# Kernel optimization log

Measured on AMD Instinct MI355X. Metric: run time of the kernel, lower is better.

## Reference

```python
import jax, jax.numpy as jnp
import numpy as np

N = 100000   # nodes
F = 512      # in_channels
H = 128      # hidden_channels
HEADS = 2
E = 1600000  # edges
C = 64       # out_channels (classes)
EPS = 1e-5
GW = 0.8     # graph_weight


def setup_inputs() -> dict:
    key = jax.random.key(0)
    ks = jax.random.split(key, 16)
    rn = lambda k, s: jax.random.normal(k, s, jnp.float32) * 0.05
    return {
        'x': jax.random.normal(ks[0], (N, F), jnp.float32),
        'edge_index': jax.random.randint(ks[1], (2, E), 0, N),
        # TransConv params
        't_fc_w': rn(ks[2], (F, H)), 't_fc_b': jnp.zeros((H,), jnp.float32),
        't_ln0_g': jnp.ones((H,), jnp.float32), 't_ln0_b': jnp.zeros((H,), jnp.float32),
        't_wq_w': rn(ks[3], (H, H * HEADS)), 't_wq_b': jnp.zeros((H * HEADS,), jnp.float32),
        't_wk_w': rn(ks[4], (H, H * HEADS)), 't_wk_b': jnp.zeros((H * HEADS,), jnp.float32),
        't_wv_w': rn(ks[5], (H, H * HEADS)), 't_wv_b': jnp.zeros((H * HEADS,), jnp.float32),
        't_ln1_g': jnp.ones((H,), jnp.float32), 't_ln1_b': jnp.zeros((H,), jnp.float32),
        # GraphConv params
        'g_fc_w': rn(ks[6], (F, H)), 'g_fc_b': jnp.zeros((H,), jnp.float32),
        'g_bn0_g': jnp.ones((H,), jnp.float32), 'g_bn0_b': jnp.zeros((H,), jnp.float32),
        'g_conv_w': rn(ks[7], (H, H)), 'g_conv_b': jnp.zeros((H,), jnp.float32),
        'g_bn1_g': jnp.ones((H,), jnp.float32), 'g_bn1_b': jnp.zeros((H,), jnp.float32),
        # output fc
        'fc_w': rn(ks[8], (H, C)), 'fc_b': jnp.zeros((C,), jnp.float32),
    }


def _layernorm(x, g, b):
    mu = jnp.mean(x, axis=-1, keepdims=True)
    var = jnp.mean((x - mu) ** 2, axis=-1, keepdims=True)
    return (x - mu) * jax.lax.rsqrt(var + EPS) * g + b


def _batchnorm_eval(x, g, b):
    # eval-mode BN right after reset: running_mean=0, running_var=1
    return x * (1.0 / np.sqrt(1.0 + EPS)) * g + b


def _trans_conv(x, fc_w, fc_b, ln0_g, ln0_b, wq_w, wq_b, wk_w, wk_b, wv_w, wv_b, ln1_g, ln1_b):
    h = jax.nn.relu(_layernorm(x @ fc_w + fc_b, ln0_g, ln0_b))
    x0 = h
    n = h.shape[0]
    qs = (h @ wq_w + wq_b).reshape(n, HEADS, H)
    ks = (h @ wk_w + wk_b).reshape(n, HEADS, H)
    vs = (h @ wv_w + wv_b).reshape(n, HEADS, H)
    # global (Frobenius) norm, as in torch.norm(qs, p=2)
    qs = qs / jnp.linalg.norm(qs)
    ks = ks / jnp.linalg.norm(ks)
    kvs = jnp.einsum('lhm,lhd->hmd', ks, vs)                  # [h, m, d]
    attention_num = jnp.einsum('nhm,hmd->nhd', qs, kvs) + n * vs
    ks_sum = jnp.sum(ks, axis=0)                              # [h, m]
    normalizer = jnp.einsum('nhm,hm->nh', qs, ks_sum)[..., None] + float(n)
    attn_out = (attention_num / normalizer).mean(axis=1)       # [n, H]
    h = (attn_out + x0) / 2.0
    h = jax.nn.relu(_layernorm(h, ln1_g, ln1_b))
    return h


def _graph_conv(x, edge_index, fc_w, fc_b, bn0_g, bn0_b, conv_w, conv_b, bn1_g, bn1_b):
    h = jax.nn.relu(_batchnorm_eval(x @ fc_w + fc_b, bn0_g, bn0_b))
    x0 = h
    row, col = edge_index[0], edge_index[1]
    n = h.shape[0]
    deg = jax.ops.segment_sum(jnp.ones((row.shape[0],), jnp.float32), col, num_segments=n)
    val = jnp.sqrt(1.0 / deg[col]) * jnp.sqrt(1.0 / deg[row])
    val = jnp.nan_to_num(val, nan=0.0, posinf=0.0, neginf=0.0)
    agg = jax.ops.segment_sum(val[:, None] * h[row], col, num_segments=n)  # [n, H]
    h2 = agg @ conv_w + conv_b
    h2 = jax.nn.relu(_batchnorm_eval(h2, bn1_g, bn1_b))
    return h2 + x0


def reference(x, edge_index,
              t_fc_w, t_fc_b, t_ln0_g, t_ln0_b, t_wq_w, t_wq_b, t_wk_w, t_wk_b,
              t_wv_w, t_wv_b, t_ln1_g, t_ln1_b,
              g_fc_w, g_fc_b, g_bn0_g, g_bn0_b, g_conv_w, g_conv_b, g_bn1_g, g_bn1_b,
              fc_w, fc_b):
    x1 = _trans_conv(x, t_fc_w, t_fc_b, t_ln0_g, t_ln0_b, t_wq_w, t_wq_b,
                     t_wk_w, t_wk_b, t_wv_w, t_wv_b, t_ln1_g, t_ln1_b)
    x2 = _graph_conv(x, edge_index, g_fc_w, g_fc_b, g_bn0_g, g_bn0_b,
                     g_conv_w, g_conv_b, g_bn1_g, g_bn1_b)
    out = GW * x2 + (1.0 - GW) * x1
    return out @ fc_w + fc_b
```

## Files before the change

kernel.cpp:

```cpp
#include <hip/hip_runtime.h>

constexpr int N = 100000;
constexpr int F = 512;
constexpr int H = 128;
constexpr int E = 1600000;
constexpr int C = 64;
constexpr float EPS = 1e-5f;
constexpr float NF = 100000.0f;
constexpr float IBN = 0.999995000037f;

constexpr size_t OFF_HT   = 0;
constexpr size_t OFF_HG   = 12800000;
constexpr size_t OFF_AGG  = 25600000;
constexpr size_t OFF_CNT  = 38400000;
constexpr size_t OFF_S    = 38500000;
constexpr size_t OFF_G    = 38500128;
constexpr size_t OFF_PTR  = 38516512;
constexpr size_t OFF_CUR  = 38616512;
constexpr size_t OFF_BS   = 38716512;
constexpr size_t OFF_SROW = 38716640;
constexpr size_t OFF_SVAL = 40316640;
constexpr size_t OFF_GWV  = 41916640;
constexpr size_t OFF_KV   = OFF_GWV + 3 * 32768;
constexpr size_t OFF_KSUM = OFF_KV + 32768;
constexpr size_t OFF_VSUM = OFF_KSUM + 256;
constexpr size_t OFF_QSUM = OFF_VSUM + 256;
constexpr size_t OFF_SC   = OFF_QSUM + 256;
constexpr size_t OFF_B    = OFF_SC + 4;
constexpr size_t OFF_CC   = OFF_B + 32768;
constexpr size_t OFF_U    = OFF_CC + 256;
constexpr size_t OFF_U0   = OFF_U + 256;
constexpr size_t OFF_BT   = OFF_U0 + 4;

constexpr int NB1024 = (N + 1023) / 1024;
constexpr int NB_GRAM = (N + 255) / 256;
constexpr size_t SP_BASE = (size_t)NB_GRAM * 16384;

typedef __attribute__((ext_vector_type(8))) short short8;
typedef __attribute__((ext_vector_type(4))) float floatx4;

__device__ __forceinline__ float4 ld4(const float* p) {
  return *reinterpret_cast<const float4*>(p);
}
__device__ __forceinline__ void st4(float* p, float4 v) {
  *reinterpret_cast<float4*>(p) = v;
}
__device__ __forceinline__ unsigned short f2bf(float f) {
  unsigned u = __float_as_uint(f);
  u += 0x7fff + ((u >> 16) & 1);
  return (unsigned short)(u >> 16);
}
__device__ __forceinline__ float bf2f(unsigned short h) {
  return __uint_as_float((unsigned)h << 16);
}

__global__ __launch_bounds__(256) void k0_cvt(const float* __restrict__ Wt,
    const float* __restrict__ Wg, unsigned short* __restrict__ Bt)
{
  const int idx = blockIdx.x * 256 + threadIdx.x;
  const int k = idx >> 8;
  const int n = idx & 255;
  float v = (n < 128) ? Wt[(size_t)k * H + n] : Wg[(size_t)k * H + (n - 128)];
  Bt[(size_t)n * F + k] = f2bf(v);
}

__global__ __launch_bounds__(256) void k1_mfma(
    const float* __restrict__ x, const unsigned short* __restrict__ Bt,
    const float* __restrict__ bt, const float* __restrict__ lng, const float* __restrict__ lnb,
    const float* __restrict__ bgv, const float* __restrict__ bng, const float* __restrict__ bnb,
    float* __restrict__ ht, float* __restrict__ hg)
{
  __shared__ __align__(16) union {
    struct { unsigned short A[64 * 72]; unsigned short B[256 * 72]; } st;
    struct { float lns[64 * 132]; float mu[64]; float rs[64]; } ln;
  } sm;
  const int t = threadIdx.x;
  const int lane = t & 63;
  const int w = t >> 6;
  const int rq = (w >> 1) * 32;
  const int cq = (w & 1) * 128;
  const int g = lane >> 4;
  const int m = lane & 15;
  const int M0 = blockIdx.x * 64;

  floatx4 acc[2][8];
#pragma unroll
  for (int rt = 0; rt < 2; ++rt)
#pragma unroll
    for (int ct = 0; ct < 8; ++ct) acc[rt][ct] = (floatx4){0.f, 0.f, 0.f, 0.f};

  const int srow = t >> 2;
  const int scol = (t & 3) * 16;
  const int grow = (M0 + srow < N) ? (M0 + srow) : (N - 1);
  const float* xp = x + (size_t)grow * F;
  const unsigned short* bsrc = Bt + (size_t)t * F;

  for (int k0 = 0; k0 < F; k0 += 64) {
#pragma unroll
    for (int j = 0; j < 4; ++j) {
      float4 a4 = ld4(xp + k0 + scol + j * 4);
      ushort4 p;
      p.x = f2bf(a4.x); p.y = f2bf(a4.y); p.z = f2bf(a4.z); p.w = f2bf(a4.w);
      *(ushort4*)(sm.st.A + srow * 72 + scol + j * 4) = p;
    }
#pragma unroll
    for (int j = 0; j < 8; ++j)
      *(uint4*)(sm.st.B + t * 72 + j * 8) = *(const uint4*)(bsrc + k0 + j * 8);
    __syncthreads();
#pragma unroll
    for (int kk = 0; kk < 64; kk += 32) {
      short8 af[2], bf[8];
#pragma unroll
      for (int rt = 0; rt < 2; ++rt)
        af[rt] = *(const short8*)(sm.st.A + (rq + rt * 16 + m) * 72 + kk + g * 8);
#pragma unroll
      for (int ct = 0; ct < 8; ++ct)
        bf[ct] = *(const short8*)(sm.st.B + (cq + ct * 16 + m) * 72 + kk + g * 8);
#pragma unroll
      for (int rt = 0; rt < 2; ++rt)
#pragma unroll
        for (int ct = 0; ct < 8; ++ct)
          acc[rt][ct] = __builtin_amdgcn_mfma_f32_16x16x32_bf16(af[rt], bf[ct], acc[rt][ct], 0, 0, 0);
    }
    __syncthreads();
  }
  if (cq == 0) {
#pragma unroll
    for (int rt = 0; rt < 2; ++rt)
#pragma unroll
      for (int ct = 0; ct < 8; ++ct) {
        const int col = ct * 16 + m;
        const float b = bt[col];
#pragma unroll
        for (int r = 0; r < 4; ++r)
          sm.ln.lns[(rq + rt * 16 + g * 4 + r) * 132 + col] = acc[rt][ct][r] + b;
      }
  } else {
#pragma unroll
    for (int rt = 0; rt < 2; ++rt)
#pragma unroll
      for (int ct = 0; ct < 8; ++ct) {
        const int col = ct * 16 + m;
        const float s1 = IBN * bng[col], b0 = bgv[col], b2 = bnb[col];
#pragma unroll
        for (int r = 0; r < 4; ++r) {
          const int row = M0 + rq + rt * 16 + g * 4 + r;
          if (row < N) {
            float v = (acc[rt][ct][r] + b0) * s1 + b2;
            hg[(size_t)row * H + col] = v > 0.f ? v : 0.f;
          }
        }
      }
  }
  __syncthreads();
  if (t < 64) {
    float sum = 0.f, sq = 0.f;
    for (int c2 = 0; c2 < H; ++c2) {
      float v = sm.ln.lns[t * 132 + c2];
      sum += v; sq += v * v;
    }
    float mu = sum * (1.f / H);
    float var = sq * (1.f / H) - mu * mu;
    sm.ln.mu[t] = mu; sm.ln.rs[t] = rsqrtf(var + EPS);
  }
  __syncthreads();
  {
    const int r = t >> 2;
    const int cb = (t & 3) * 32;
    if (M0 + r < N) {
      const float mu = sm.ln.mu[r], rs = sm.ln.rs[r];
#pragma unroll
      for (int j = 0; j < 8; ++j) {
        const int c = cb + j * 4;
        float o[4];
#pragma unroll
        for (int q = 0; q < 4; ++q) {
          float v = (sm.ln.lns[r * 132 + c + q] - mu) * rs * lng[c + q] + lnb[c + q];
          o[q] = v > 0.f ? v : 0.f;
        }
        st4(ht + (size_t)(M0 + r) * H + c, make_float4(o[0], o[1], o[2], o[3]));
      }
    }
  }
}

__global__ __launch_bounds__(256) void k2_gram(const float* __restrict__ ht,
                                               float* __restrict__ gp,
                                               float* __restrict__ sp)
{
  const int t = threadIdx.x;
  const int b = blockIdx.x;
  const int base = b * 256;
  const int nend = (base + 256 < N) ? base + 256 : N;
  const int r0 = (t >> 4) * 8;
  const int c0 = (t & 15) * 8;
  float acc[8][8] = {};
  float colacc[8] = {};
  const bool do_col = (t < 16);
  int n = base;
  for (; n + 1 < nend; n += 2) {
    const float* hp0 = ht + (size_t)n * H;
    const float* hp1 = hp0 + H;
    float4 a00 = ld4(hp0 + r0), a01 = ld4(hp0 + r0 + 4);
    float4 b00 = ld4(hp0 + c0), b01 = ld4(hp0 + c0 + 4);
    float4 a10 = ld4(hp1 + r0), a11 = ld4(hp1 + r0 + 4);
    float4 b10 = ld4(hp1 + c0), b11 = ld4(hp1 + c0 + 4);
    float a0[8] = {a00.x, a00.y, a00.z, a00.w, a01.x, a01.y, a01.z, a01.w};
    float b0[8] = {b00.x, b00.y, b00.z, b00.w, b01.x, b01.y, b01.z, b01.w};
    float a1[8] = {a10.x, a10.y, a10.z, a10.w, a11.x, a11.y, a11.z, a11.w};
    float b1[8] = {b10.x, b10.y, b10.z, b10.w, b11.x, b11.y, b11.z, b11.w};
    if (do_col) {
#pragma unroll
      for (int j = 0; j < 8; ++j) colacc[j] += b0[j] + b1[j];
    }
#pragma unroll
    for (int i = 0; i < 8; ++i)
#pragma unroll
      for (int j = 0; j < 8; ++j)
        acc[i][j] += a0[i] * b0[j] + a1[i] * b1[j];
  }
  if (n < nend) {
    const float* hp0 = ht + (size_t)n * H;
    float4 a00 = ld4(hp0 + r0), a01 = ld4(hp0 + r0 + 4);
    float4 b00 = ld4(hp0 + c0), b01 = ld4(hp0 + c0 + 4);
    float a0[8] = {a00.x, a00.y, a00.z, a00.w, a01.x, a01.y, a01.z, a01.w};
    float b0[8] = {b00.x, b00.y, b00.z, b00.w, b01.x, b01.y, b01.z, b01.w};
    if (do_col) {
#pragma unroll
      for (int j = 0; j < 8; ++j) colacc[j] += b0[j];
    }
#pragma unroll
    for (int i = 0; i < 8; ++i)
#pragma unroll
      for (int j = 0; j < 8; ++j)
        acc[i][j] += a0[i] * b0[j];
  }
  float* g = gp + (size_t)b * 16384;
#pragma unroll
  for (int i = 0; i < 8; ++i) {
    st4(&g[(r0 + i) * H + c0], make_float4(acc[i][0], acc[i][1], acc[i][2], acc[i][3]));
    st4(&g[(r0 + i) * H + c0 + 4], make_float4(acc[i][4], acc[i][5], acc[i][6], acc[i][7]));
  }
  if (do_col) {
    float* spb = sp + (size_t)b * 128;
    st4(&spb[c0], make_float4(colacc[0], colacc[1], colacc[2], colacc[3]));
    st4(&spb[c0 + 4], make_float4(colacc[4], colacc[5], colacc[6], colacc[7]));
  }
}

__global__ __launch_bounds__(256) void k2r_reduce(const float* __restrict__ gp,
    const float* __restrict__ sp, float* __restrict__ G, float* __restrict__ s)
{
  const int i = blockIdx.x * 256 + threadIdx.x;
  float s0 = 0.f, s1 = 0.f, s2 = 0.f, s3 = 0.f;
  int b = 0;
  for (; b + 3 < NB_GRAM; b += 4) {
    s0 += gp[(size_t)b * 16384 + i];
    s1 += gp[(size_t)(b + 1) * 16384 + i];
    s2 += gp[(size_t)(b + 2) * 16384 + i];
    s3 += gp[(size_t)(b + 3) * 16384 + i];
  }
  for (; b < NB_GRAM; ++b) s0 += gp[(size_t)b * 16384 + i];
  G[i] = (s0 + s1) + (s2 + s3);
  if (blockIdx.x == 0 && threadIdx.x < 128) {
    float t0 = 0.f, t1 = 0.f;
    int bb = 0;
    for (; bb + 1 < NB_GRAM; bb += 2) {
      t0 += sp[(size_t)bb * 128 + threadIdx.x];
      t1 += sp[(size_t)(bb + 1) * 128 + threadIdx.x];
    }
    for (; bb < NB_GRAM; ++bb) t0 += sp[(size_t)bb * 128 + threadIdx.x];
    s[threadIdx.x] = t0 + t1;
  }
}

__global__ __launch_bounds__(256) void k3a_gw(const float* __restrict__ G,
    const float* __restrict__ Wv, const float* __restrict__ Wk,
    const float* __restrict__ Wq, float* __restrict__ GW)
{
  const int flat = blockIdx.x * 256 + threadIdx.x;
  const int w = flat >> 15;
  const int rem = flat & 32767;
  const int i = rem >> 8;
  const int j = rem & 255;
  const float* W = (w == 0) ? Wv : (w == 1) ? Wk : Wq;
  float sum = 0.f;
#pragma unroll 8
  for (int k = 0; k < H; ++k) sum += G[i * H + k] * W[k * 256 + j];
  GW[flat] = sum;
}

__global__ __launch_bounds__(256) void k3k_sums(const float* __restrict__ s,
    const float* __restrict__ Wk, const float* __restrict__ bk,
    const float* __restrict__ Wv, const float* __restrict__ bv,
    const float* __restrict__ Wq, const float* __restrict__ bq,
    float* __restrict__ ksum, float* __restrict__ vsum, float* __restrict__ qsum)
{
  const int flat = blockIdx.x * 256 + threadIdx.x;
  const int w = flat >> 8;
  const int j = flat & 255;
  const float* W = (w == 0) ? Wk : (w == 1) ? Wv : Wq;
  const float* b = (w == 0) ? bk : (w == 1) ? bv : bq;
  float* out = (w == 0) ? ksum : (w == 1) ? vsum : qsum;
  float sum = 0.f;
#pragma unroll 8
  for (int k = 0; k < H; ++k) sum += s[k] * W[k * 256 + j];
  out[j] = sum + NF * b[j];
}

__global__ __launch_bounds__(256) void k3b_kv(const float* __restrict__ GWv,
    const float* __restrict__ s, const float* __restrict__ Wk,
    const float* __restrict__ bk, const float* __restrict__ bv,
    const float* __restrict__ vsum, float* __restrict__ kv)
{
  const int flat = blockIdx.x * 256 + threadIdx.x;
  const int h = flat >> 14;
  const int m = (flat >> 7) & 127;
  const int d = flat & 127;
  float s1 = 0.f, s2 = 0.f;
#pragma unroll 4
  for (int k = 0; k < H; ++k) {
    float wkv = Wk[k * 256 + h * 128 + m];
    s1 += wkv * GWv[k * 256 + h * 128 + d];
    s2 += wkv * s[k];
  }
  kv[flat] = s1 + s2 * bv[h * 128 + d] + bk[h * 128 + m] * vsum[h * 128 + d];
}

__global__ __launch_bounds__(256) void k3c_ssq(
    const float* __restrict__ Wk, const float* __restrict__ GWk,
    const float* __restrict__ Wq, const float* __restrict__ GWq,
    const float* __restrict__ bk, const float* __restrict__ ksum,
    const float* __restrict__ bq, const float* __restrict__ qsum,
    float* __restrict__ sc)
{
  __shared__ float red[512];
  const int t = threadIdx.x;
  float pk = 0.f, pq = 0.f;
  for (int i = t; i < 32768; i += 256) {
    pk += Wk[i] * GWk[i];
    pq += Wq[i] * GWq[i];
  }
  pk += 2.f * bk[t] * ksum[t] - NF * bk[t] * bk[t];
  pq += 2.f * bq[t] * qsum[t] - NF * bq[t] * bq[t];
  red[t] = pk; red[256 + t] = pq;
  __syncthreads();
  for (int off = 128; off > 0; off >>= 1) {
    if (t < off) { red[t] += red[t + off]; red[256 + t] += red[256 + t + off]; }
    __syncthreads();
  }
  if (t == 0) {
    float ssq_k = red[0], ssq_q = red[256];
    sc[0] = ssq_q; sc[1] = ssq_k;
    sc[2] = rsqrtf(ssq_q * ssq_k);
  }
}

__global__ __launch_bounds__(256) void k3d_B(const float* __restrict__ Wq,
    const float* __restrict__ kv, const float* __restrict__ Wv,
    const float* __restrict__ sc, unsigned short* __restrict__ Bt2)
{
  const int flat = blockIdx.x * 256 + threadIdx.x;
  const int i = flat >> 8;
  const int j = flat & 255;
  const int h = j >> 7;
  const int d = j & 127;
  const float inv = sc[2];
  float sum = 0.f;
#pragma unroll 4
  for (int m = 0; m < H; ++m)
    sum += Wq[i * 256 + h * 128 + m] * kv[h * 16384 + m * 128 + d];
  Bt2[(size_t)j * H + i] = f2bf(sum * inv + NF * Wv[i * 256 + j]);
}

__global__ __launch_bounds__(512) void k3e_small(const float* __restrict__ bq,
    const float* __restrict__ kv, const float* __restrict__ bv,
    const float* __restrict__ Wq, const float* __restrict__ ksum,
    const float* __restrict__ sc, float* __restrict__ cc,
    float* __restrict__ u, float* __restrict__ u0)
{
  const int t = threadIdx.x;
  const float inv = sc[2];
  if (t < 256) {
    const int h = t >> 7, d = t & 127;
    float sum = 0.f;
    for (int m = 0; m < H; ++m) sum += bq[h * 128 + m] * kv[h * 16384 + m * 128 + d];
    cc[t] = sum * inv + NF * bv[t];
  } else {
    const int q = t - 256;
    const int i = q >> 1, h = q & 1;
    float sum = 0.f;
    for (int m = 0; m < H; ++m) sum += Wq[i * 256 + h * 128 + m] * ksum[h * 128 + m];
    u[i * 2 + h] = sum * inv;
  }
  if (t < 2) {
    float sum = 0.f;
    for (int m = 0; m < H; ++m) sum += bq[t * 128 + m] * ksum[t * 128 + m];
    u0[t] = sum * inv + NF;
  }
}

__global__ __launch_bounds__(256) void k4_mfma(float* __restrict__ ht,
    const unsigned short* __restrict__ Bt2, const float* __restrict__ cc,
    const float* __restrict__ u, const float* __restrict__ u0,
    const float* __restrict__ lng, const float* __restrict__ lnb)
{
  __shared__ __align__(16) union {
    unsigned short A[64 * 136];
    float lns[64 * 132];
  } sm;
  __shared__ float u_s[256];
  __shared__ float rden_s[128];
  __shared__ float mu_s[64], rs_s[64];
  const int t = threadIdx.x;
  const int lane = t & 63;
  const int w = t >> 6;
  const int rq = w * 16;
  const int g = lane >> 4;
  const int m = lane & 15;
  const int M0 = blockIdx.x * 64;

  {
    const int srow = t >> 2;
    const int scol = (t & 3) * 32;
    const int grow = (M0 + srow < N) ? (M0 + srow) : (N - 1);
    const float* xp = ht + (size_t)grow * H + scol;
#pragma unroll
    for (int j = 0; j < 8; ++j) {
      float4 a4 = ld4(xp + j * 4);
      ushort4 p;
      p.x = f2bf(a4.x); p.y = f2bf(a4.y); p.z = f2bf(a4.z); p.w = f2bf(a4.w);
      *(ushort4*)(sm.A + srow * 136 + scol + j * 4) = p;
    }
  }
  u_s[t] = u[t];
  __syncthreads();

  floatx4 acc[16];
#pragma unroll
  for (int ct = 0; ct < 16; ++ct) acc[ct] = (floatx4){0.f, 0.f, 0.f, 0.f};
#pragma unroll
  for (int kk = 0; kk < 128; kk += 32) {
    short8 af = *(const short8*)(sm.A + (rq + m) * 136 + kk + g * 8);
#pragma unroll
    for (int ct = 0; ct < 16; ++ct) {
      short8 bf = *(const short8*)(Bt2 + (size_t)(ct * 16 + m) * H + kk + g * 8);
      acc[ct] = __builtin_amdgcn_mfma_f32_16x16x32_bf16(af, bf, acc[ct], 0, 0, 0);
    }
  }
  if (t < 128) {
    const int row = t >> 1, head = t & 1;
    float den = u0[head];
    for (int k = 0; k < H; ++k)
      den += bf2f(sm.A[row * 136 + k]) * u_s[k * 2 + head];
    rden_s[row * 2 + head] = 0.5f / den;
  }
  __syncthreads();

#pragma unroll
  for (int ct = 0; ct < 8; ++ct) {
    const int d = ct * 16 + m;
    const float c0v = cc[d], c1v = cc[128 + d];
#pragma unroll
    for (int r = 0; r < 4; ++r) {
      const int row = rq + g * 4 + r;
      const int grow = M0 + row;
      const float rd0 = rden_s[row * 2], rd1 = rden_s[row * 2 + 1];
      float attn = (acc[ct][r] + c0v) * rd0 + (acc[ct + 8][r] + c1v) * rd1;
      float hres = (grow < N) ? ht[(size_t)grow * H + d] : 0.f;
      sm.lns[row * 132 + d] = (attn + hres) * 0.5f;
    }
  }
  __syncthreads();
  if (t < 64) {
    float sum = 0.f, sq = 0.f;
    for (int c2 = 0; c2 < H; ++c2) {
      float v = sm.lns[t * 132 + c2];
      sum += v; sq += v * v;
    }
    float mu = sum * (1.f / H);
    float var = sq * (1.f / H) - mu * mu;
    mu_s[t] = mu; rs_s[t] = rsqrtf(var + EPS);
  }
  __syncthreads();
  {
    const int r = t >> 2;
    const int cb = (t & 3) * 32;
    if (M0 + r < N) {
      const float mu = mu_s[r], rs = rs_s[r];
#pragma unroll
      for (int j = 0; j < 8; ++j) {
        const int c = cb + j * 4;
        float o[4];
#pragma unroll
        for (int q = 0; q < 4; ++q) {
          float v = (sm.lns[r * 132 + c + q] - mu) * rs * lng[c + q] + lnb[c + q];
          o[q] = v > 0.f ? v : 0.f;
        }
        st4(ht + (size_t)(M0 + r) * H + c, make_float4(o[0], o[1], o[2], o[3]));
      }
    }
  }
}

__global__ __launch_bounds__(256) void k5_deg(const int* __restrict__ ei,
                                              int* __restrict__ cnt)
{
  const int i = blockIdx.x * 256 + threadIdx.x;
  if (i < E) atomicAdd(&cnt[ei[E + i]], 1);
}

__global__ __launch_bounds__(256) void k_scan1(const int* __restrict__ cnt,
                                               int* __restrict__ bsum)
{
  __shared__ int red[256];
  const int t = threadIdx.x;
  const int base = blockIdx.x * 1024 + t * 4;
  int s = 0;
#pragma unroll
  for (int j = 0; j < 4; ++j) {
    int idx = base + j;
    if (idx < N) s += cnt[idx];
  }
  red[t] = s;
  __syncthreads();
  for (int off = 128; off > 0; off >>= 1) {
    if (t < off) red[t] += red[t + off];
    __syncthreads();
  }
  if (t == 0) bsum[blockIdx.x] = red[0];
}

__global__ void k_scan2(int* __restrict__ bsum)
{
  if (threadIdx.x == 0 && blockIdx.x == 0) {
    int run = 0;
    for (int b = 0; b < NB1024; ++b) {
      int v = bsum[b];
      bsum[b] = run;
      run += v;
    }
  }
}

__global__ __launch_bounds__(256) void k_scan3(const int* __restrict__ cnt,
    const int* __restrict__ bsum, int* __restrict__ ptr, int* __restrict__ cur)
{
  __shared__ int part[256];
  const int t = threadIdx.x;
  const int base = blockIdx.x * 1024 + t * 4;
  int v[4];
  int tsum = 0;
#pragma unroll
  for (int j = 0; j < 4; ++j) {
    int idx = base + j;
    v[j] = (idx < N) ? cnt[idx] : 0;
    tsum += v[j];
  }
  part[t] = tsum;
  __syncthreads();
  for (int off = 1; off < 256; off <<= 1) {
    int add = (t >= off) ? part[t - off] : 0;
    __syncthreads();
    part[t] += add;
    __syncthreads();
  }
  int run = bsum[blockIdx.x] + part[t] - tsum;
#pragma unroll
  for (int j = 0; j < 4; ++j) {
    int idx = base + j;
    if (idx < N) { ptr[idx] = run; cur[idx] = run; }
    run += v[j];
  }
}

__global__ __launch_bounds__(256) void k6a_place(const int* __restrict__ ei,
    const int* __restrict__ cnt, int* __restrict__ cur,
    int* __restrict__ srow, float* __restrict__ sval)
{
  const int e = blockIdx.x * 256 + threadIdx.x;
  if (e >= E) return;
  const int r = ei[e];
  const int c = ei[E + e];
  const int p = atomicAdd(&cur[c], 1);
  srow[p] = r;
  const int dr = cnt[r];
  const float dv = (float)dr * (float)cnt[c];
  sval[p] = (dr > 0) ? rsqrtf(dv) : 0.f;
}

__global__ __launch_bounds__(256) void k6b_gather(const int* __restrict__ ptr,
    const int* __restrict__ cnt, const int* __restrict__ srow,
    const float* __restrict__ sval, const float* __restrict__ hg,
    float* __restrict__ agg)
{
  const int t = threadIdx.x;
  const int n = blockIdx.x * 8 + (t >> 5);
  const int lane4 = (t & 31) * 4;
  const int start = ptr[n];
  const int end = start + cnt[n];
  float4 acc = make_float4(0.f, 0.f, 0.f, 0.f);
  int e = start;
  for (; e + 1 < end; e += 2) {
    int r0 = srow[e], r1 = srow[e + 1];
    float v0 = sval[e], v1 = sval[e + 1];
    float4 h0 = ld4(hg + (size_t)r0 * H + lane4);
    float4 h1 = ld4(hg + (size_t)r1 * H + lane4);
    acc.x += v0 * h0.x + v1 * h1.x;
    acc.y += v0 * h0.y + v1 * h1.y;
    acc.z += v0 * h0.z + v1 * h1.z;
    acc.w += v0 * h0.w + v1 * h1.w;
  }
  if (e < end) {
    int r0 = srow[e];
    float v0 = sval[e];
    float4 h0 = ld4(hg + (size_t)r0 * H + lane4);
    acc.x += v0 * h0.x;
    acc.y += v0 * h0.y;
    acc.z += v0 * h0.z;
    acc.w += v0 * h0.w;
  }
  st4(agg + (size_t)n * H + lane4, acc);
}

__global__ __launch_bounds__(256) void k7_conv(const float* __restrict__ agg,
    float* __restrict__ hg, const float* __restrict__ Wc,
    const float* __restrict__ cb, const float* __restrict__ g1,
    const float* __restrict__ b1)
{
  const int t = threadIdx.x;
  const int R0 = blockIdx.x * 32;
  const int r0 = (t >> 5) * 4;
  const int c0 = (t & 31) * 4;
  float acc[4][4] = {};
  for (int k0 = 0; k0 < H; k0 += 4) {
    float ax[4][4];
#pragma unroll
    for (int r = 0; r < 4; ++r) {
      float4 a4 = ld4(agg + (size_t)(R0 + r0 + r) * H + k0);
      ax[r][0] = a4.x; ax[r][1] = a4.y; ax[r][2] = a4.z; ax[r][3] = a4.w;
    }
#pragma unroll
    for (int kk = 0; kk < 4; ++kk) {
      float4 w = ld4(Wc + (size_t)(k0 + kk) * H + c0);
#pragma unroll
      for (int r = 0; r < 4; ++r) {
        float av = ax[r][kk];
        acc[r][0] += av * w.x; acc[r][1] += av * w.y;
        acc[r][2] += av * w.z; acc[r][3] += av * w.w;
      }
    }
  }
#pragma unroll
  for (int r = 0; r < 4; ++r) {
    size_t off = (size_t)(R0 + r0 + r) * H + c0;
    float4 res = ld4(hg + off);
    float rsv[4] = {res.x, res.y, res.z, res.w};
    float o[4];
#pragma unroll
    for (int j = 0; j < 4; ++j) {
      float v = (acc[r][j] + cb[c0 + j]) * IBN * g1[c0 + j] + b1[c0 + j];
      v = v > 0.f ? v : 0.f;
      o[j] = v + rsv[j];
    }
    st4(hg + off, make_float4(o[0], o[1], o[2], o[3]));
  }
}

__global__ __launch_bounds__(256) void k8_out(const float* __restrict__ ht,
    const float* __restrict__ hg, const float* __restrict__ W,
    const float* __restrict__ bias, float* __restrict__ out)
{
  const int t = threadIdx.x;
  const int R0 = blockIdx.x * 32;
  const int rr0 = (t >> 4) * 2;
  const int c0 = (t & 15) * 4;
  float acc[2][4] = {};
  for (int k0 = 0; k0 < H; k0 += 4) {
    float ax[2][4];
#pragma unroll
    for (int r = 0; r < 2; ++r) {
      size_t off = (size_t)(R0 + rr0 + r) * H + k0;
      float4 a1 = ld4(ht + off);
      float4 a2 = ld4(hg + off);
      ax[r][0] = 0.2f * a1.x + 0.8f * a2.x;
      ax[r][1] = 0.2f * a1.y + 0.8f * a2.y;
      ax[r][2] = 0.2f * a1.z + 0.8f * a2.z;
      ax[r][3] = 0.2f * a1.w + 0.8f * a2.w;
    }
#pragma unroll
    for (int kk = 0; kk < 4; ++kk) {
      float4 w = ld4(W + (size_t)(k0 + kk) * C + c0);
#pragma unroll
      for (int r = 0; r < 2; ++r) {
        float av = ax[r][kk];
        acc[r][0] += av * w.x; acc[r][1] += av * w.y;
        acc[r][2] += av * w.z; acc[r][3] += av * w.w;
      }
    }
  }
#pragma unroll
  for (int r = 0; r < 2; ++r) {
    float o[4];
#pragma unroll
    for (int j = 0; j < 4; ++j) o[j] = acc[r][j] + bias[c0 + j];
    st4(out + (size_t)(R0 + rr0 + r) * C + c0, make_float4(o[0], o[1], o[2], o[3]));
  }
}

extern "C" void kernel_launch(void* const* d_in, const int* in_sizes, int n_in,
                              void* d_out, int out_size, void* d_ws, size_t ws_size,
                              hipStream_t stream) {
  (void)in_sizes; (void)n_in; (void)out_size; (void)ws_size;
  const float* x       = (const float*)d_in[0];
  const int*   ei      = (const int*)d_in[1];
  const float* t_fc_w  = (const float*)d_in[2];
  const float* t_fc_b  = (const float*)d_in[3];
  const float* t_ln0_g = (const float*)d_in[4];
  const float* t_ln0_b = (const float*)d_in[5];
  const float* t_wq_w  = (const float*)d_in[6];
  const float* t_wq_b  = (const float*)d_in[7];
  const float* t_wk_w  = (const float*)d_in[8];
  const float* t_wk_b  = (const float*)d_in[9];
  const float* t_wv_w  = (const float*)d_in[10];
  const float* t_wv_b  = (const float*)d_in[11];
  const float* t_ln1_g = (const float*)d_in[12];
  const float* t_ln1_b = (const float*)d_in[13];
  const float* g_fc_w  = (const float*)d_in[14];
  const float* g_fc_b  = (const float*)d_in[15];
  const float* g_bn0_g = (const float*)d_in[16];
  const float* g_bn0_b = (const float*)d_in[17];
  const float* g_cv_w  = (const float*)d_in[18];
  const float* g_cv_b  = (const float*)d_in[19];
  const float* g_bn1_g = (const float*)d_in[20];
  const float* g_bn1_b = (const float*)d_in[21];
  const float* fc_w    = (const float*)d_in[22];
  const float* fc_b    = (const float*)d_in[23];

  float* W    = (float*)d_ws;
  float* ht   = W + OFF_HT;
  float* hg   = W + OFF_HG;
  float* agg  = W + OFF_AGG;
  int*   cnt  = (int*)(W + OFF_CNT);
  float* s    = W + OFF_S;
  float* G    = W + OFF_G;
  int*   ptr  = (int*)(W + OFF_PTR);
  int*   cur  = (int*)(W + OFF_CUR);
  int*   bsum = (int*)(W + OFF_BS);
  int*   srow = (int*)(W + OFF_SROW);
  float* sval = W + OFF_SVAL;
  float* gw   = W + OFF_GWV;
  float* kv   = W + OFF_KV;
  float* ksum = W + OFF_KSUM;
  float* vsum = W + OFF_VSUM;
  float* qsum = W + OFF_QSUM;
  float* sc   = W + OFF_SC;
  unsigned short* Bt2 = (unsigned short*)(W + OFF_B);
  float* cc   = W + OFF_CC;
  float* u    = W + OFF_U;
  float* u0   = W + OFF_U0;
  unsigned short* Bt = (unsigned short*)(W + OFF_BT);

  hipMemsetAsync(cnt, 0, N * sizeof(int), stream);

  k0_cvt<<<512, 256, 0, stream>>>(t_fc_w, g_fc_w, Bt);

  k5_deg<<<(E + 255) / 256, 256, 0, stream>>>(ei, cnt);
  k_scan1<<<NB1024, 256, 0, stream>>>(cnt, bsum);
  k_scan2<<<1, 64, 0, stream>>>(bsum);
  k_scan3<<<NB1024, 256, 0, stream>>>(cnt, bsum, ptr, cur);
  k6a_place<<<E / 256, 256, 0, stream>>>(ei, cnt, cur, srow, sval);

  k1_mfma<<<(N + 63) / 64, 256, 0, stream>>>(x, Bt, t_fc_b, t_ln0_g, t_ln0_b,
                                             g_fc_b, g_bn0_g, g_bn0_b, ht, hg);
  k2_gram<<<NB_GRAM, 256, 0, stream>>>(ht, agg, agg + SP_BASE);
  k2r_reduce<<<64, 256, 0, stream>>>(agg, agg + SP_BASE, G, s);
  k6b_gather<<<N / 8, 256, 0, stream>>>(ptr, cnt, srow, sval, hg, agg);
  k3a_gw<<<384, 256, 0, stream>>>(G, t_wv_w, t_wk_w, t_wq_w, gw);
  k3k_sums<<<3, 256, 0, stream>>>(s, t_wk_w, t_wk_b, t_wv_w, t_wv_b, t_wq_w, t_wq_b,
                                  ksum, vsum, qsum);
  k3b_kv<<<128, 256, 0, stream>>>(gw, s, t_wk_w, t_wk_b, t_wv_b, vsum, kv);
  k3c_ssq<<<1, 256, 0, stream>>>(t_wk_w, gw + 32768, t_wq_w, gw + 65536,
                                 t_wk_b, ksum, t_wq_b, qsum, sc);
  k3d_B<<<128, 256, 0, stream>>>(t_wq_w, kv, t_wv_w, sc, Bt2);
  k3e_small<<<1, 512, 0, stream>>>(t_wq_b, kv, t_wv_b, t_wq_w, ksum, sc, cc, u, u0);
  k4_mfma<<<(N + 63) / 64, 256, 0, stream>>>(ht, Bt2, cc, u, u0, t_ln1_g, t_ln1_b);
  k7_conv<<<N / 32, 256, 0, stream>>>(agg, hg, g_cv_w, g_cv_b, g_bn1_g, g_bn1_b);
  k8_out<<<N / 32, 256, 0, stream>>>(ht, hg, fc_w, fc_b, (float*)d_out);
}
```

Baseline: 1.200 ms.

## Rewrite input GEMM without LDS: per-wave register tiles and shuffle-based LayerNorm

The fused x@[Wt|Wg] GEMM no longer stages A and B tiles through shared memory with block barriers. Each wave now owns 32 rows and all 256 output columns. It loads x directly into registers with a one-step prefetch and reads bf16 weight fragments straight from global/L2. LayerNorm statistics are computed with cross-lane xor shuffles instead of a single-thread shared-memory pass, and blocks cover 128 rows. This removes barrier and LDS traffic plus a serial LN reduction, but raises register pressure (128 accumulator floats) and re-reads the weights from cache per wave.

```diff
diff --git a/kernel.cpp b/kernel.cpp
--- a/kernel.cpp
+++ b/kernel.cpp
@@ -53,6 +53,14 @@
 __device__ __forceinline__ float bf2f(unsigned short h) {
   return __uint_as_float((unsigned)h << 16);
 }
+__device__ __forceinline__ short8 pack8(float4 a, float4 b) {
+  short8 r;
+  r[0] = (short)f2bf(a.x); r[1] = (short)f2bf(a.y);
+  r[2] = (short)f2bf(a.z); r[3] = (short)f2bf(a.w);
+  r[4] = (short)f2bf(b.x); r[5] = (short)f2bf(b.y);
+  r[6] = (short)f2bf(b.z); r[7] = (short)f2bf(b.w);
+  return r;
+}
 
 __global__ __launch_bounds__(256) void k0_cvt(const float* __restrict__ Wt,
     const float* __restrict__ Wg, unsigned short* __restrict__ Bt)
@@ -70,115 +78,95 @@
     const float* __restrict__ bgv, const float* __restrict__ bng, const float* __restrict__ bnb,
     float* __restrict__ ht, float* __restrict__ hg)
 {
-  __shared__ __align__(16) union {
-    struct { unsigned short A[64 * 72]; unsigned short B[256 * 72]; } st;
-    struct { float lns[64 * 132]; float mu[64]; float rs[64]; } ln;
-  } sm;
   const int t = threadIdx.x;
   const int lane = t & 63;
   const int w = t >> 6;
-  const int rq = (w >> 1) * 32;
-  const int cq = (w & 1) * 128;
   const int g = lane >> 4;
   const int m = lane & 15;
-  const int M0 = blockIdx.x * 64;
-
-  floatx4 acc[2][8];
+  const int M0 = blockIdx.x * 128 + w * 32;
+
+  const int r0 = M0 + m;
+  const int r1 = M0 + 16 + m;
+  const float* xp0 = x + (size_t)(r0 < N ? r0 : N - 1) * F + g * 8;
+  const float* xp1 = x + (size_t)(r1 < N ? r1 : N - 1) * F + g * 8;
+
+  floatx4 acc[2][16];
 #pragma unroll
   for (int rt = 0; rt < 2; ++rt)
 #pragma unroll
-    for (int ct = 0; ct < 8; ++ct) acc[rt][ct] = (floatx4){0.f, 0.f, 0.f, 0.f};
-
-  const int srow = t >> 2;
-  const int scol = (t & 3) * 16;
-  const int grow = (M0 + srow < N) ? (M0 + srow) : (N - 1);
-  const float* xp = x + (size_t)grow * F;
-  const unsigned short* bsrc = Bt + (size_t)t * F;
-
-  for (int k0 = 0; k0 < F; k0 += 64) {
-#pragma unroll
-    for (int j = 0; j < 4; ++j) {
-      float4 a4 = ld4(xp + k0 + scol + j * 4);
-      ushort4 p;
-      p.x = f2bf(a4.x); p.y = f2bf(a4.y); p.z = f2bf(a4.z); p.w = f2bf(a4.w);
-      *(ushort4*)(sm.st.A + srow * 72 + scol + j * 4) = p;
-    }
-#pragma unroll
-    for (int j = 0; j < 8; ++j)
-      *(uint4*)(sm.st.B + t * 72 + j * 8) = *(const uint4*)(bsrc + k0 + j * 8);
-    __syncthreads();
-#pragma unroll
-    for (int kk = 0; kk < 64; kk += 32) {
-      short8 af[2], bf[8];
-#pragma unroll
-      for (int rt = 0; rt < 2; ++rt)
-        af[rt] = *(const short8*)(sm.st.A + (rq + rt * 16 + m) * 72 + kk + g * 8);
-#pragma unroll
-      for (int ct = 0; ct < 8; ++ct)
-        bf[ct] = *(const short8*)(sm.st.B + (cq + ct * 16 + m) * 72 + kk + g * 8);
-#pragma unroll
-      for (int rt = 0; rt < 2; ++rt)
-#pragma unroll
-        for (int ct = 0; ct < 8; ++ct)
-          acc[rt][ct] = __builtin_amdgcn_mfma_f32_16x16x32_bf16(af[rt], bf[ct], acc[rt][ct], 0, 0, 0);
-    }
-    __syncthreads();
-  }
-  if (cq == 0) {
-#pragma unroll
-    for (int rt = 0; rt < 2; ++rt)
+    for (int ct = 0; ct < 16; ++ct) acc[rt][ct] = (floatx4){0.f, 0.f, 0.f, 0.f};
+
+  float4 pa0 = ld4(xp0), pa1 = ld4(xp0 + 4);
+  float4 pa2 = ld4(xp1), pa3 = ld4(xp1 + 4);
+
+  const unsigned short* bp0 = Bt + (size_t)m * F + g * 8;
+
+#pragma unroll 2
+  for (int kk = 0; kk < F; kk += 32) {
+    short8 af0 = pack8(pa0, pa1);
+    short8 af1 = pack8(pa2, pa3);
+    if (kk + 32 < F) {
+      pa0 = ld4(xp0 + kk + 32); pa1 = ld4(xp0 + kk + 36);
+      pa2 = ld4(xp1 + kk + 32); pa3 = ld4(xp1 + kk + 36);
+    }
+    const unsigned short* bp = bp0 + kk;
+#pragma unroll
+    for (int ct = 0; ct < 16; ++ct) {
+      short8 bf = *(const short8*)(bp + (size_t)ct * 16 * F);
+      acc[0][ct] = __builtin_amdgcn_mfma_f32_16x16x32_bf16(af0, bf, acc[0][ct], 0, 0, 0);
+      acc[1][ct] = __builtin_amdgcn_mfma_f32_16x16x32_bf16(af1, bf, acc[1][ct], 0, 0, 0);
+    }
+  }
+
+  float bt_l[8], lng_l[8], lnb_l[8];
+#pragma unroll
+  for (int ct = 0; ct < 8; ++ct) {
+    bt_l[ct] = bt[ct * 16 + m];
+    lng_l[ct] = lng[ct * 16 + m];
+    lnb_l[ct] = lnb[ct * 16 + m];
+  }
+#pragma unroll
+  for (int rt = 0; rt < 2; ++rt) {
+#pragma unroll
+    for (int r = 0; r < 4; ++r) {
+      float sum = 0.f, sq = 0.f;
 #pragma unroll
       for (int ct = 0; ct < 8; ++ct) {
-        const int col = ct * 16 + m;
-        const float b = bt[col];
-#pragma unroll
-        for (int r = 0; r < 4; ++r)
-          sm.ln.lns[(rq + rt * 16 + g * 4 + r) * 132 + col] = acc[rt][ct][r] + b;
+        float v = acc[rt][ct][r] + bt_l[ct];
+        acc[rt][ct][r] = v;
+        sum += v; sq += v * v;
       }
-  } else {
-#pragma unroll
-    for (int rt = 0; rt < 2; ++rt)
-#pragma unroll
-      for (int ct = 0; ct < 8; ++ct) {
-        const int col = ct * 16 + m;
-        const float s1 = IBN * bng[col], b0 = bgv[col], b2 = bnb[col];
-#pragma unroll
-        for (int r = 0; r < 4; ++r) {
-          const int row = M0 + rq + rt * 16 + g * 4 + r;
-          if (row < N) {
-            float v = (acc[rt][ct][r] + b0) * s1 + b2;
-            hg[(size_t)row * H + col] = v > 0.f ? v : 0.f;
-          }
+#pragma unroll
+      for (int off = 1; off < 16; off <<= 1) {
+        sum += __shfl_xor(sum, off, 64);
+        sq  += __shfl_xor(sq,  off, 64);
+      }
+      const float mu = sum * (1.f / H);
+      const float rs = rsqrtf(sq * (1.f / H) - mu * mu + EPS);
+      const int row = M0 + rt * 16 + g * 4 + r;
+      if (row < N) {
+        float* hp = ht + (size_t)row * H + m;
+#pragma unroll
+        for (int ct = 0; ct < 8; ++ct) {
+          float o = (acc[rt][ct][r] - mu) * rs * lng_l[ct] + lnb_l[ct];
+          hp[ct * 16] = o > 0.f ? o : 0.f;
         }
       }
-  }
-  __syncthreads();
-  if (t < 64) {
-    float sum = 0.f, sq = 0.f;
-    for (int c2 = 0; c2 < H; ++c2) {
-      float v = sm.ln.lns[t * 132 + c2];
-      sum += v; sq += v * v;
-    }
-    float mu = sum * (1.f / H);
-    float var = sq * (1.f / H) - mu * mu;
-    sm.ln.mu[t] = mu; sm.ln.rs[t] = rsqrtf(var + EPS);
-  }
-  __syncthreads();
-  {
-    const int r = t >> 2;
-    const int cb = (t & 3) * 32;
-    if (M0 + r < N) {
-      const float mu = sm.ln.mu[r], rs = sm.ln.rs[r];
-#pragma unroll
-      for (int j = 0; j < 8; ++j) {
-        const int c = cb + j * 4;
-        float o[4];
-#pragma unroll
-        for (int q = 0; q < 4; ++q) {
-          float v = (sm.ln.lns[r * 132 + c + q] - mu) * rs * lng[c + q] + lnb[c + q];
-          o[q] = v > 0.f ? v : 0.f;
+    }
+  }
+#pragma unroll
+  for (int ct = 8; ct < 16; ++ct) {
+    const int c2 = (ct - 8) * 16 + m;
+    const float s1 = IBN * bng[c2], b0 = bgv[c2], b2 = bnb[c2];
+#pragma unroll
+    for (int rt = 0; rt < 2; ++rt) {
+#pragma unroll
+      for (int r = 0; r < 4; ++r) {
+        const int row = M0 + rt * 16 + g * 4 + r;
+        if (row < N) {
+          float v = (acc[rt][ct][r] + b0) * s1 + b2;
+          hg[(size_t)row * H + c2] = v > 0.f ? v : 0.f;
         }
-        st4(ht + (size_t)(M0 + r) * H + c, make_float4(o[0], o[1], o[2], o[3]));
       }
     }
   }
@@ -771,8 +759,8 @@
   k_scan3<<<NB1024, 256, 0, stream>>>(cnt, bsum, ptr, cur);
   k6a_place<<<E / 256, 256, 0, stream>>>(ei, cnt, cur, srow, sval);
 
-  k1_mfma<<<(N + 63) / 64, 256, 0, stream>>>(x, Bt, t_fc_b, t_ln0_g, t_ln0_b,
-                                             g_fc_b, g_bn0_g, g_bn0_b, ht, hg);
+  k1_mfma<<<(N + 127) / 128, 256, 0, stream>>>(x, Bt, t_fc_b, t_ln0_g, t_ln0_b,
+                                               g_fc_b, g_bn0_g, g_bn0_b, ht, hg);
   k2_gram<<<NB_GRAM, 256, 0, stream>>>(ht, agg, agg + SP_BASE);
   k2r_reduce<<<64, 256, 0, stream>>>(agg, agg + SP_BASE, G, s);
   k6b_gather<<<N / 8, 256, 0, stream>>>(ptr, cnt, srow, sval, hg, agg);
```

Result: slower. 1.272 ms (+6.0%).

## Prefetch next K-tile into registers and reorder bf16 weight layout for coalescing

Applied to the files above, without the earlier changes.

The weight-conversion kernel now writes the bf16 weight matrix in a tiled layout (k-tile, 8-element chunk, column). This lets each thread fetch its per-tile B slice with coalesced uint4 loads across the block. The GEMM main loop becomes software pipelined: the next K-tile of x and B is loaded into registers while MFMAs run on the current shared-memory tile, then written to shared memory after a barrier. The aim is to hide global load latency in the first projection GEMM, at the cost of more registers, which may lower occupancy.

```diff
diff --git a/kernel.cpp b/kernel.cpp
--- a/kernel.cpp
+++ b/kernel.cpp
@@ -61,7 +61,10 @@
   const int k = idx >> 8;
   const int n = idx & 255;
   float v = (n < 128) ? Wt[(size_t)k * H + n] : Wg[(size_t)k * H + (n - 128)];
-  Bt[(size_t)n * F + k] = f2bf(v);
+  const int kt = k >> 6;
+  const int j  = (k >> 3) & 7;
+  const int e  = k & 7;
+  Bt[((size_t)((kt * 8 + j) * 256 + n) << 3) + e] = f2bf(v);
 }
 
 __global__ __launch_bounds__(256) void k1_mfma(
@@ -92,21 +95,37 @@
   const int srow = t >> 2;
   const int scol = (t & 3) * 16;
   const int grow = (M0 + srow < N) ? (M0 + srow) : (N - 1);
-  const float* xp = x + (size_t)grow * F;
-  const unsigned short* bsrc = Bt + (size_t)t * F;
-
-  for (int k0 = 0; k0 < F; k0 += 64) {
+  const float* xp = x + (size_t)grow * F + scol;
+  const uint4* btg = (const uint4*)Bt;
+
+  float4 ar[4];
+  uint4  br[8];
+
+#pragma unroll
+  for (int j = 0; j < 4; ++j) ar[j] = ld4(xp + j * 4);
+#pragma unroll
+  for (int j = 0; j < 8; ++j) br[j] = btg[j * 256 + t];
+  {
 #pragma unroll
     for (int j = 0; j < 4; ++j) {
-      float4 a4 = ld4(xp + k0 + scol + j * 4);
       ushort4 p;
-      p.x = f2bf(a4.x); p.y = f2bf(a4.y); p.z = f2bf(a4.z); p.w = f2bf(a4.w);
+      p.x = f2bf(ar[j].x); p.y = f2bf(ar[j].y); p.z = f2bf(ar[j].z); p.w = f2bf(ar[j].w);
       *(ushort4*)(sm.st.A + srow * 72 + scol + j * 4) = p;
     }
 #pragma unroll
     for (int j = 0; j < 8; ++j)
-      *(uint4*)(sm.st.B + t * 72 + j * 8) = *(const uint4*)(bsrc + k0 + j * 8);
-    __syncthreads();
+      *(uint4*)(sm.st.B + t * 72 + j * 8) = br[j];
+  }
+  __syncthreads();
+
+  for (int kt = 0; kt < 8; ++kt) {
+    if (kt + 1 < 8) {
+      const int kb = (kt + 1) * 64;
+#pragma unroll
+      for (int j = 0; j < 4; ++j) ar[j] = ld4(xp + kb + j * 4);
+#pragma unroll
+      for (int j = 0; j < 8; ++j) br[j] = btg[((kt + 1) * 8 + j) * 256 + t];
+    }
 #pragma unroll
     for (int kk = 0; kk < 64; kk += 32) {
       short8 af[2], bf[8];
@@ -123,7 +142,20 @@
           acc[rt][ct] = __builtin_amdgcn_mfma_f32_16x16x32_bf16(af[rt], bf[ct], acc[rt][ct], 0, 0, 0);
     }
     __syncthreads();
-  }
+    if (kt + 1 < 8) {
+#pragma unroll
+      for (int j = 0; j < 4; ++j) {
+        ushort4 p;
+        p.x = f2bf(ar[j].x); p.y = f2bf(ar[j].y); p.z = f2bf(ar[j].z); p.w = f2bf(ar[j].w);
+        *(ushort4*)(sm.st.A + srow * 72 + scol + j * 4) = p;
+      }
+#pragma unroll
+      for (int j = 0; j < 8; ++j)
+        *(uint4*)(sm.st.B + t * 72 + j * 8) = br[j];
+      __syncthreads();
+    }
+  }
+
   if (cq == 0) {
 #pragma unroll
     for (int rt = 0; rt < 2; ++rt)
```

New measurement: 1.277 ms. 6.4% more time.

## Double-buffer k1 GEMM staging with direct global-to-LDS loads and swizzled B layout

Applied to the files above, without the earlier changes.

The first GEMM kernel now walks K in 32-wide steps with double-buffered LDS for A and B, so loads of the next tile are issued before the MFMAs on the current one. B is pre-packed by k0_cvt into a swizzled, chunked layout and copied straight into LDS with global_load_lds, which skips register staging and is meant to avoid LDS bank conflicts. Launch bounds now request 3 blocks per CU. The price is twice as many barriers per K (16 steps instead of 8) and more complex indexing. The bigger LDS footprint and the occupancy hint could also raise register pressure.

```diff
diff --git a/kernel.cpp b/kernel.cpp
--- a/kernel.cpp
+++ b/kernel.cpp
@@ -53,6 +53,11 @@
 __device__ __forceinline__ float bf2f(unsigned short h) {
   return __uint_as_float((unsigned)h << 16);
 }
+__device__ __forceinline__ void gl_lds16(const unsigned short* g, unsigned short* l) {
+  __builtin_amdgcn_global_load_lds(
+      (const __attribute__((address_space(1))) unsigned int*)g,
+      (__attribute__((address_space(3))) unsigned int*)l, 16, 0, 0);
+}
 
 __global__ __launch_bounds__(256) void k0_cvt(const float* __restrict__ Wt,
     const float* __restrict__ Wg, unsigned short* __restrict__ Bt)
@@ -61,17 +66,21 @@
   const int k = idx >> 8;
   const int n = idx & 255;
   float v = (n < 128) ? Wt[(size_t)k * H + n] : Wg[(size_t)k * H + (n - 128)];
-  Bt[(size_t)n * F + k] = f2bf(v);
-}
-
-__global__ __launch_bounds__(256) void k1_mfma(
+  const int kt = k >> 5;
+  const int g  = (k >> 3) & 3;
+  const int e  = k & 7;
+  const int chunk = g * 256 + ((n + 2 * g) & 255);
+  Bt[(((size_t)kt * 1024 + chunk) << 3) + e] = f2bf(v);
+}
+
+__global__ __launch_bounds__(256, 3) void k1_mfma(
     const float* __restrict__ x, const unsigned short* __restrict__ Bt,
     const float* __restrict__ bt, const float* __restrict__ lng, const float* __restrict__ lnb,
     const float* __restrict__ bgv, const float* __restrict__ bng, const float* __restrict__ bnb,
     float* __restrict__ ht, float* __restrict__ hg)
 {
   __shared__ __align__(16) union {
-    struct { unsigned short A[64 * 72]; unsigned short B[256 * 72]; } st;
+    struct { unsigned short A[2][64 * 40]; unsigned short B[2][8192]; } st;
     struct { float lns[64 * 132]; float mu[64]; float rs[64]; } ln;
   } sm;
   const int t = threadIdx.x;
@@ -90,40 +99,67 @@
     for (int ct = 0; ct < 8; ++ct) acc[rt][ct] = (floatx4){0.f, 0.f, 0.f, 0.f};
 
   const int srow = t >> 2;
-  const int scol = (t & 3) * 16;
+  const int scol8 = (t & 3) * 8;
   const int grow = (M0 + srow < N) ? (M0 + srow) : (N - 1);
-  const float* xp = x + (size_t)grow * F;
-  const unsigned short* bsrc = Bt + (size_t)t * F;
-
-  for (int k0 = 0; k0 < F; k0 += 64) {
-#pragma unroll
-    for (int j = 0; j < 4; ++j) {
-      float4 a4 = ld4(xp + k0 + scol + j * 4);
-      ushort4 p;
-      p.x = f2bf(a4.x); p.y = f2bf(a4.y); p.z = f2bf(a4.z); p.w = f2bf(a4.w);
-      *(ushort4*)(sm.st.A + srow * 72 + scol + j * 4) = p;
-    }
-#pragma unroll
-    for (int j = 0; j < 8; ++j)
-      *(uint4*)(sm.st.B + t * 72 + j * 8) = *(const uint4*)(bsrc + k0 + j * 8);
-    __syncthreads();
-#pragma unroll
-    for (int kk = 0; kk < 64; kk += 32) {
+  const float* xp = x + (size_t)grow * F + scol8;
+
+  const int mb = cq + m + 2 * g;
+
+  {
+#pragma unroll
+    for (int i = 0; i < 4; ++i)
+      gl_lds16(Bt + (((size_t)(i * 256 + t)) << 3),
+               &sm.st.B[0][(size_t)(i * 256 + (w << 6)) << 3]);
+    float4 a0 = ld4(xp), a1 = ld4(xp + 4);
+    ushort4 p0, p1;
+    p0.x = f2bf(a0.x); p0.y = f2bf(a0.y); p0.z = f2bf(a0.z); p0.w = f2bf(a0.w);
+    p1.x = f2bf(a1.x); p1.y = f2bf(a1.y); p1.z = f2bf(a1.z); p1.w = f2bf(a1.w);
+    *(ushort4*)(sm.st.A[0] + srow * 40 + scol8) = p0;
+    *(ushort4*)(sm.st.A[0] + srow * 40 + scol8 + 4) = p1;
+  }
+  __syncthreads();
+
+#pragma unroll 2
+  for (int kt = 0; kt < 16; ++kt) {
+    const int cur = kt & 1, nxt = cur ^ 1;
+    float4 a0, a1;
+    const bool more = (kt + 1 < 16);
+    if (more) {
+#pragma unroll
+      for (int i = 0; i < 4; ++i)
+        gl_lds16(Bt + (((size_t)(kt + 1) * 1024 + i * 256 + t) << 3),
+                 &sm.st.B[nxt][(size_t)(i * 256 + (w << 6)) << 3]);
+      a0 = ld4(xp + (kt + 1) * 32);
+      a1 = ld4(xp + (kt + 1) * 32 + 4);
+    }
+    {
+      const unsigned short* Ab = sm.st.A[cur];
+      const unsigned short* Bb = sm.st.B[cur];
       short8 af[2], bf[8];
 #pragma unroll
       for (int rt = 0; rt < 2; ++rt)
-        af[rt] = *(const short8*)(sm.st.A + (rq + rt * 16 + m) * 72 + kk + g * 8);
-#pragma unroll
-      for (int ct = 0; ct < 8; ++ct)
-        bf[ct] = *(const short8*)(sm.st.B + (cq + ct * 16 + m) * 72 + kk + g * 8);
+        af[rt] = *(const short8*)(Ab + (rq + rt * 16 + m) * 40 + g * 8);
+#pragma unroll
+      for (int ct = 0; ct < 8; ++ct) {
+        const int chunk = g * 256 + ((mb + ct * 16) & 255);
+        bf[ct] = *(const short8*)(Bb + ((size_t)chunk << 3));
+      }
 #pragma unroll
       for (int rt = 0; rt < 2; ++rt)
 #pragma unroll
         for (int ct = 0; ct < 8; ++ct)
           acc[rt][ct] = __builtin_amdgcn_mfma_f32_16x16x32_bf16(af[rt], bf[ct], acc[rt][ct], 0, 0, 0);
     }
+    if (more) {
+      ushort4 p0, p1;
+      p0.x = f2bf(a0.x); p0.y = f2bf(a0.y); p0.z = f2bf(a0.z); p0.w = f2bf(a0.w);
+      p1.x = f2bf(a1.x); p1.y = f2bf(a1.y); p1.z = f2bf(a1.z); p1.w = f2bf(a1.w);
+      *(ushort4*)(sm.st.A[nxt] + srow * 40 + scol8) = p0;
+      *(ushort4*)(sm.st.A[nxt] + srow * 40 + scol8 + 4) = p1;
+    }
     __syncthreads();
   }
+
   if (cq == 0) {
 #pragma unroll
     for (int rt = 0; rt < 2; ++rt)
```

New measurement: 1.172 ms. 2.3% less time.
